# Kernel tuning notes

Hardware: AMD Instinct MI355X
Metric: run time of the kernel (lower is better)

The kernel has to match this reference:

```python
import jax, jax.numpy as jnp
import numpy as np

B = 8192
NUM_SAMPLES = 128
RESAMPLE_PADDING = 0.01
F32_EPS = float(np.finfo(np.float32).eps)


def lift_gaussian_diag(d, t_mean, t_var, r_var):
    # d: [B,3]; t_mean/t_var/r_var: [B,S]
    mean = d[..., None, :] * t_mean[..., None]                      # [B,S,3]
    d_mag_sq = jnp.clip(jnp.sum(d ** 2, axis=-1, keepdims=True), 1e-10)
    d_outer_diag = d ** 2
    null_outer_diag = 1.0 - d_outer_diag / d_mag_sq
    cov_diag = (t_var[..., None] * d_outer_diag[..., None, :]
                + r_var[..., None] * null_outer_diag[..., None, :])  # [B,S,3]
    return mean, cov_diag


def conical_frustum_to_gaussian(d, t0, t1, base_radius):
    # stable=True branch of the original code
    mu = (t0 + t1) / 2
    hw = (t1 - t0) / 2
    t_mean = mu + 2 * mu * hw ** 2 / (3 * mu ** 2 + hw ** 2)
    t_var = hw ** 2 / 3 - 4 / 15 * (hw ** 4 * (12 * mu ** 2 - hw ** 2)
                                    / (3 * mu ** 2 + hw ** 2) ** 2)
    r_var = base_radius ** 2 * (mu ** 2 / 4 + 5 / 12 * hw ** 2
                                - 4 / 15 * hw ** 4 / (3 * mu ** 2 + hw ** 2))
    return lift_gaussian_diag(d, t_mean, t_var, r_var)


def cast_rays(t_vals, origins, directions, radii):
    # ray_shape == 'cone', diag == True
    means, covs = conical_frustum_to_gaussian(
        directions, t_vals[..., :-1], t_vals[..., 1:], radii)
    return means + origins[..., None, :], covs


def sorted_piecewise_constant_pdf(bins, weights, num_samples):
    # randomized=False branch; faithful O(n*m) mask-based interval search
    eps = 1e-5
    weight_sum = jnp.sum(weights, axis=-1, keepdims=True)
    padding = jnp.clip(eps - weight_sum, 0)
    weights = weights + padding / weights.shape[-1]
    weight_sum = weight_sum + padding
    pdf = weights / weight_sum
    cdf = jnp.minimum(jnp.cumsum(pdf[..., :-1], axis=-1), 1.0)
    z = jnp.zeros(cdf.shape[:-1] + (1,), cdf.dtype)
    o = jnp.ones(cdf.shape[:-1] + (1,), cdf.dtype)
    cdf = jnp.concatenate([z, cdf, o], axis=-1)                      # [B, nb+1]
    u = jnp.linspace(0.0, 1.0 - F32_EPS, num_samples, dtype=cdf.dtype)
    u = jnp.broadcast_to(u, cdf.shape[:-1] + (num_samples,))         # [B, S]
    mask = u[..., None, :] >= cdf[..., :, None]                      # [B, nb+1, S]

    def find_interval(x):
        x0 = jnp.max(jnp.where(mask, x[..., None], x[..., :1, None]), axis=-2)
        x1 = jnp.min(jnp.where(~mask, x[..., None], x[..., -1:, None]), axis=-2)
        return x0, x1

    bins_g0, bins_g1 = find_interval(bins)
    cdf_g0, cdf_g1 = find_interval(cdf)
    t = jnp.clip(jnp.nan_to_num((u - cdf_g0) / (cdf_g1 - cdf_g0)), 0, 1)
    return bins_g0 + t * (bins_g1 - bins_g0)


def setup_inputs() -> dict:
    key = jax.random.key(0)
    k0, k1, k2, k3 = jax.random.split(key, 4)
    origins = jax.random.normal(k0, (B, 3), dtype=jnp.float32)
    directions = jax.random.normal(k1, (B, 3), dtype=jnp.float32)
    directions = directions / jnp.linalg.norm(directions, axis=-1, keepdims=True)
    radii = 0.001 + 0.01 * jax.random.uniform(k2, (B, 1), dtype=jnp.float32)
    near = 2.0 * jnp.ones((B, 1), dtype=jnp.float32)
    far = 6.0 * jnp.ones((B, 1), dtype=jnp.float32)
    weights = jax.random.uniform(k3, (B, NUM_SAMPLES), dtype=jnp.float32)
    return {"origins": origins, "directions": directions, "radii": radii,
            "near": near, "far": far, "weights": weights}


def reference(origins, directions, radii, near, far, weights):
    # coarse stratified sampling (randomized=False, lindisp=False)
    t = jnp.linspace(0.0, 1.0, NUM_SAMPLES + 1, dtype=jnp.float32)
    t_coarse = near * (1.0 - t) + far * t                            # [B, S+1]
    means_c, covs_c = cast_rays(t_coarse, origins, directions, radii)
    # resample_along_rays: blur weights then inverse-CDF sample
    wpad = jnp.concatenate([weights[..., :1], weights, weights[..., -1:]], axis=-1)
    wmax = jnp.maximum(wpad[..., :-1], wpad[..., 1:])
    wblur = 0.5 * (wmax[..., :-1] + wmax[..., 1:]) + RESAMPLE_PADDING
    t_fine = sorted_piecewise_constant_pdf(t_coarse, wblur, t_coarse.shape[-1])
    means_f, covs_f = cast_rays(t_fine, origins, directions, radii)
    return (t_coarse, means_c, covs_c, t_fine, means_f, covs_f)
```

## Files before the change

### kernel.cpp

```cpp
#include <hip/hip_runtime.h>


constexpr int B_RAYS = 8192;
constexpr int S      = 128;
constexpr int SP1    = 129;
constexpr float F32_EPS = 1.1920928955078125e-07f;
constexpr float USTEP   = (1.0f - F32_EPS) / 128.0f;
constexpr float R_SCALE = 128.0f / (1.0f - F32_EPS);

constexpr long long O_TC = 0;
constexpr long long O_MC = O_TC + (long long)B_RAYS * SP1;
constexpr long long O_CC = O_MC + (long long)B_RAYS * S * 3;
constexpr long long O_TF = O_CC + (long long)B_RAYS * S * 3;
constexpr long long O_MF = O_TF + (long long)B_RAYS * SP1;
constexpr long long O_CF = O_MF + (long long)B_RAYS * S * 3;

typedef float vf4 __attribute__((ext_vector_type(4)));

__device__ __forceinline__ float frcp(float x) { return __builtin_amdgcn_rcpf(x); }

template<int CTRL, int RM>
__device__ __forceinline__ float dpp_addf(float x) {
    int m = __builtin_amdgcn_update_dpp(0, __builtin_bit_cast(int, x),
                                        CTRL, RM, 0xF, true);
    return x + __builtin_bit_cast(float, m);
}
template<int CTRL>
__device__ __forceinline__ float dpp_movf(float x) {
    int m = __builtin_amdgcn_update_dpp(0, __builtin_bit_cast(int, x),
                                        CTRL, 0xF, 0xF, true);
    return __builtin_bit_cast(float, m);
}

__device__ __forceinline__ void st_nt(float* p, float v) {
    __builtin_nontemporal_store(v, p);
}
__device__ __forceinline__ void st_nt4(float* p, float4 v) {
    __builtin_nontemporal_store(__builtin_bit_cast(vf4, v),
                                reinterpret_cast<vf4*>(p));
}

__device__ __forceinline__ void frustum(float t0, float t1, float rad2,
                                        float& tm, float& tv, float& rv)
{
    float mu  = 0.5f * (t0 + t1);
    float hw  = 0.5f * (t1 - t0);
    float mu2 = mu * mu, hw2 = hw * hw, hw4 = hw2 * hw2;
    float den  = fmaf(3.0f, mu2, hw2);
    float rden = frcp(den);
    tm = fmaf(2.0f * mu * hw2, rden, mu);
    tv = hw2 * (1.0f / 3.0f)
       - (4.0f / 15.0f) * (hw4 * fmaf(12.0f, mu2, -hw2)) * (rden * rden);
    rv = rad2 * (0.25f * mu2 + (5.0f / 12.0f) * hw2 - (4.0f / 15.0f) * hw4 * rden);
}

__device__ __forceinline__ float sel3(int c, float x, float y, float z)
{
    return (c == 0) ? x : ((c == 1) ? y : z);
}

__device__ __forceinline__ int smin_of(float c)
{
    int s = (int)ceilf(c * R_SCALE);
    s = s < 0 ? 0 : (s > 129 ? 129 : s);
    #pragma unroll
    for (int it = 0; it < 2; ++it)
        if (s > 0 && (float)(s - 1) * USTEP >= c) --s;
    #pragma unroll
    for (int it = 0; it < 2; ++it)
        if (s < 129 && (float)s * USTEP < c) ++s;
    return s;
}

__global__ __launch_bounds__(256) void mipnerf_kernel(
    const float* __restrict__ origins,
    const float* __restrict__ directions,
    const float* __restrict__ radii,
    const float* __restrict__ nearp,
    const float* __restrict__ farp,
    const float* __restrict__ weights,
    float* __restrict__ out)
{
    const int tid = threadIdx.x;
    const int w   = tid >> 6;
    const int l   = tid & 63;
    const int b   = (blockIdx.x << 2) + w;

    __shared__ float4 s_pay[4][132];
    __shared__ float4 s_fr[4][128];

    const float2 wv = *reinterpret_cast<const float2*>(weights + (long long)b * S + 2*l);
    const float ox = origins[3*b+0], oy = origins[3*b+1], oz = origins[3*b+2];
    const float dx = directions[3*b+0], dy = directions[3*b+1], dz = directions[3*b+2];
    const float rad = radii[b];
    const float nv = nearp[b], fv = farp[b];

    const float rad2   = rad * rad;
    const float axx = dx*dx, ayy = dy*dy, azz = dz*dz;
    const float dmag2  = fmaxf(axx + ayy + azz, 1e-10f);
    const float rdmag2 = frcp(dmag2);
    const float nxx = 1.0f - axx * rdmag2;
    const float nyy = 1.0f - ayy * rdmag2;
    const float nzz = 1.0f - azz * rdmag2;

    auto bin = [&](int k) {
        float t = (float)k * (1.0f / 128.0f);
        return nv * (1.0f - t) + fv * t;
    };

    {
        float* ot = out + O_TC + (long long)b * SP1;
        st_nt(ot + l,      bin(l));
        st_nt(ot + l + 64, bin(l + 64));
        if (l == 0) st_nt(ot + 128, bin(128));
    }

    #pragma unroll
    for (int j = 0; j < 2; ++j) {
        int i = l + 64*j;
        float tm, tv, rv;
        frustum(bin(i), bin(i + 1), rad2, tm, tv, rv);
        s_fr[w][i] = make_float4(tm, tv, rv, 0.0f);
    }
    __builtin_amdgcn_wave_barrier();

    auto emit_span = [&](int m, float* __restrict__ om, float* __restrict__ oc) {
        int k0 = m + m / 3;
        int r  = 4*m - 3*k0;
        float4 fA = s_fr[w][k0], fB = s_fr[w][k0 + 1];
        float4 mv, cv;
        #pragma unroll
        for (int e = 0; e < 4; ++e) {
            int  rc   = r + e;
            bool useB = rc >= 3;
            int  c    = useB ? rc - 3 : rc;
            float tm = useB ? fB.x : fA.x;
            float tv = useB ? fB.y : fA.y;
            float rv = useB ? fB.z : fA.z;
            (&mv.x)[e] = sel3(c, dx, dy, dz) * tm + sel3(c, ox, oy, oz);
            (&cv.x)[e] = tv * sel3(c, axx, ayy, azz) + rv * sel3(c, nxx, nyy, nzz);
        }
        st_nt4(om + 4*m, mv);
        st_nt4(oc + 4*m, cv);
    };

    {
        float* om = out + O_MC + (long long)b * 384;
        float* oc = out + O_CC + (long long)b * 384;
        emit_span(l, om, oc);
        if (l < 32) emit_span(l + 64, om, oc);
    }

    float wprev = dpp_movf<0x138>(wv.y);  if (l == 0)  wprev = wv.x;
    float wnext = dpp_movf<0x130>(wv.x);  if (l == 63) wnext = wv.y;
    float m0 = fmaxf(wprev, wv.x), m1 = fmaxf(wv.x, wv.y), m2 = fmaxf(wv.y, wnext);
    float wb0 = 0.5f * (m0 + m1) + 0.01f;
    float wb1 = 0.5f * (m1 + m2) + 0.01f;

    float ps = wb0 + wb1;
    float x  = ps;
    x = dpp_addf<0x111, 0xF>(x);
    x = dpp_addf<0x112, 0xF>(x);
    x = dpp_addf<0x114, 0xF>(x);
    x = dpp_addf<0x118, 0xF>(x);
    x = dpp_addf<0x142, 0xA>(x);
    x = dpp_addf<0x143, 0xC>(x);
    float incl  = x;
    float total = __builtin_bit_cast(float,
        __builtin_amdgcn_readlane(__builtin_bit_cast(int, incl), 63));

    float pad   = fmaxf(1e-5f - total, 0.0f);
    float wstot = total + pad;
    float inv   = frcp(wstot);
    float padk  = pad * (1.0f / 128.0f);
    float excl  = incl - ps;

    float Bv = fminf((excl + wb0 + (float)(2*l + 1) * padk) * inv, 1.0f);
    float Cv = (l == 63) ? 1.0f
             : fminf((incl + (float)(2*l + 2) * padk) * inv, 1.0f);
    float Av = dpp_movf<0x138>(Cv);

    int sm0 = smin_of(Av);
    int sm1 = smin_of(Bv);
    int sm2 = smin_of(Cv);
    {
        float4 payA = make_float4(Av, Bv - Av, bin(2*l),     bin(2*l + 1));
        float4 payB = make_float4(Bv, Cv - Bv, bin(2*l + 1), bin(2*l + 2));
        for (int s2 = sm0; s2 < sm1; ++s2) s_pay[w][s2] = payA;
        for (int s2 = sm1; s2 < sm2; ++s2) s_pay[w][s2] = payB;
    }
    __builtin_amdgcn_wave_barrier();

    auto sample_one = [&](int s) -> float {
        float4 p = s_pay[w][s];
        float u  = (float)s * USTEP;
        float tt = (u - p.x) * frcp(p.y);
        if (!(tt == tt)) tt = 0.0f;
        tt = fminf(fmaxf(tt, 0.0f), 1.0f);
        return p.z + tt * (p.w - p.z);
    };
    float tf0 = sample_one(l);
    float tf1 = sample_one(l + 64);
    float tf2 = sample_one(128);
    {
        float* ot = out + O_TF + (long long)b * SP1;
        st_nt(ot + l,      tf0);
        st_nt(ot + l + 64, tf1);
        if (l == 0) st_nt(ot + 128, tf2);
    }

    float tf1_0 = __builtin_bit_cast(float,
        __builtin_amdgcn_readfirstlane(__builtin_bit_cast(int, tf1)));
    float tA1 = dpp_movf<0x130>(tf0);  if (l == 63) tA1 = tf1_0;
    float tB1 = dpp_movf<0x130>(tf1);  if (l == 63) tB1 = tf2;
    {
        float tm, tv, rv;
        frustum(tf0, tA1, rad2, tm, tv, rv);
        s_fr[w][l] = make_float4(tm, tv, rv, 0.0f);
        frustum(tf1, tB1, rad2, tm, tv, rv);
        s_fr[w][l + 64] = make_float4(tm, tv, rv, 0.0f);
    }
    __builtin_amdgcn_wave_barrier();

    {
        float* om = out + O_MF + (long long)b * 384;
        float* oc = out + O_CF + (long long)b * 384;
        emit_span(l, om, oc);
        if (l < 32) emit_span(l + 64, om, oc);
    }
}

extern "C" void kernel_launch(void* const* d_in, const int* in_sizes, int n_in,
                              void* d_out, int out_size, void* d_ws, size_t ws_size,
                              hipStream_t stream)
{
    const float* origins    = (const float*)d_in[0];
    const float* directions = (const float*)d_in[1];
    const float* radii      = (const float*)d_in[2];
    const float* nearp      = (const float*)d_in[3];
    const float* farp       = (const float*)d_in[4];
    const float* weights    = (const float*)d_in[5];
    float* out = (float*)d_out;

    mipnerf_kernel<<<B_RAYS / 4, 256, 0, stream>>>(
        origins, directions, radii, nearp, farp, weights, out);
}
```

Measured before the change: 17.34 us.

## Recompute frustum moments per output span instead of staging through LDS

Drops the s_fr shared-memory staging of per-interval frustum moments. Each lane now recomputes the two frustum moments it needs from bin values (coarse) or from payload lookups via tf_of (fine). This removes LDS writes and reads and two wave barriers. Av is computed directly instead of taken from a DPP shift, and the coarse output is moved after the CDF computation. The cost is redundant frustum arithmetic and repeated s_pay reads and reciprocals for fine samples.

```diff
diff --git a/kernel.cpp b/kernel.cpp
--- a/kernel.cpp
+++ b/kernel.cpp
@@ -87,7 +87,6 @@
     const int b   = (blockIdx.x << 2) + w;
 
     __shared__ float4 s_pay[4][132];
-    __shared__ float4 s_fr[4][128];
 
     const float2 wv = *reinterpret_cast<const float2*>(weights + (long long)b * S + 2*l);
     const float ox = origins[3*b+0], oy = origins[3*b+1], oz = origins[3*b+2];
@@ -113,42 +112,6 @@
         st_nt(ot + l,      bin(l));
         st_nt(ot + l + 64, bin(l + 64));
         if (l == 0) st_nt(ot + 128, bin(128));
-    }
-
-    #pragma unroll
-    for (int j = 0; j < 2; ++j) {
-        int i = l + 64*j;
-        float tm, tv, rv;
-        frustum(bin(i), bin(i + 1), rad2, tm, tv, rv);
-        s_fr[w][i] = make_float4(tm, tv, rv, 0.0f);
-    }
-    __builtin_amdgcn_wave_barrier();
-
-    auto emit_span = [&](int m, float* __restrict__ om, float* __restrict__ oc) {
-        int k0 = m + m / 3;
-        int r  = 4*m - 3*k0;
-        float4 fA = s_fr[w][k0], fB = s_fr[w][k0 + 1];
-        float4 mv, cv;
-        #pragma unroll
-        for (int e = 0; e < 4; ++e) {
-            int  rc   = r + e;
-            bool useB = rc >= 3;
-            int  c    = useB ? rc - 3 : rc;
-            float tm = useB ? fB.x : fA.x;
-            float tv = useB ? fB.y : fA.y;
-            float rv = useB ? fB.z : fA.z;
-            (&mv.x)[e] = sel3(c, dx, dy, dz) * tm + sel3(c, ox, oy, oz);
-            (&cv.x)[e] = tv * sel3(c, axx, ayy, azz) + rv * sel3(c, nxx, nyy, nzz);
-        }
-        st_nt4(om + 4*m, mv);
-        st_nt4(oc + 4*m, cv);
-    };
-
-    {
-        float* om = out + O_MC + (long long)b * 384;
-        float* oc = out + O_CC + (long long)b * 384;
-        emit_span(l, om, oc);
-        if (l < 32) emit_span(l + 64, om, oc);
     }
 
     float wprev = dpp_movf<0x138>(wv.y);  if (l == 0)  wprev = wv.x;
@@ -175,10 +138,11 @@
     float padk  = pad * (1.0f / 128.0f);
     float excl  = incl - ps;
 
+    float Av = (l == 0)  ? 0.0f
+             : fminf((excl + (float)(2*l) * padk) * inv, 1.0f);
     float Bv = fminf((excl + wb0 + (float)(2*l + 1) * padk) * inv, 1.0f);
     float Cv = (l == 63) ? 1.0f
              : fminf((incl + (float)(2*l + 2) * padk) * inv, 1.0f);
-    float Av = dpp_movf<0x138>(Cv);
 
     int sm0 = smin_of(Av);
     int sm1 = smin_of(Bv);
@@ -191,7 +155,42 @@
     }
     __builtin_amdgcn_wave_barrier();
 
-    auto sample_one = [&](int s) -> float {
+    auto emit_span = [&](int m, float t0, float t1, float t2,
+                         float* __restrict__ om, float* __restrict__ oc) {
+        float tmA, tvA, rvA, tmB, tvB, rvB;
+        frustum(t0, t1, rad2, tmA, tvA, rvA);
+        frustum(t1, t2, rad2, tmB, tvB, rvB);
+        int k0 = m + m / 3;
+        int r  = 4*m - 3*k0;
+        float4 mv, cv;
+        #pragma unroll
+        for (int e = 0; e < 4; ++e) {
+            int  rc   = r + e;
+            bool useB = rc >= 3;
+            int  c    = useB ? rc - 3 : rc;
+            float tm = useB ? tmB : tmA;
+            float tv = useB ? tvB : tvA;
+            float rv = useB ? rvB : rvA;
+            (&mv.x)[e] = sel3(c, dx, dy, dz) * tm + sel3(c, ox, oy, oz);
+            (&cv.x)[e] = tv * sel3(c, axx, ayy, azz) + rv * sel3(c, nxx, nyy, nzz);
+        }
+        st_nt4(om + 4*m, mv);
+        st_nt4(oc + 4*m, cv);
+    };
+
+    {
+        float* om = out + O_MC + (long long)b * 384;
+        float* oc = out + O_CC + (long long)b * 384;
+        int k0 = l + l / 3;
+        emit_span(l, bin(k0), bin(k0 + 1), bin(k0 + 2), om, oc);
+        if (l < 32) {
+            int m2s = l + 64;
+            int k0b = m2s + m2s / 3;
+            emit_span(m2s, bin(k0b), bin(k0b + 1), bin(k0b + 2), om, oc);
+        }
+    }
+
+    auto tf_of = [&](int s) -> float {
         float4 p = s_pay[w][s];
         float u  = (float)s * USTEP;
         float tt = (u - p.x) * frcp(p.y);
@@ -199,34 +198,23 @@
         tt = fminf(fmaxf(tt, 0.0f), 1.0f);
         return p.z + tt * (p.w - p.z);
     };
-    float tf0 = sample_one(l);
-    float tf1 = sample_one(l + 64);
-    float tf2 = sample_one(128);
     {
         float* ot = out + O_TF + (long long)b * SP1;
-        st_nt(ot + l,      tf0);
-        st_nt(ot + l + 64, tf1);
-        if (l == 0) st_nt(ot + 128, tf2);
-    }
-
-    float tf1_0 = __builtin_bit_cast(float,
-        __builtin_amdgcn_readfirstlane(__builtin_bit_cast(int, tf1)));
-    float tA1 = dpp_movf<0x130>(tf0);  if (l == 63) tA1 = tf1_0;
-    float tB1 = dpp_movf<0x130>(tf1);  if (l == 63) tB1 = tf2;
-    {
-        float tm, tv, rv;
-        frustum(tf0, tA1, rad2, tm, tv, rv);
-        s_fr[w][l] = make_float4(tm, tv, rv, 0.0f);
-        frustum(tf1, tB1, rad2, tm, tv, rv);
-        s_fr[w][l + 64] = make_float4(tm, tv, rv, 0.0f);
-    }
-    __builtin_amdgcn_wave_barrier();
+        st_nt(ot + l,      tf_of(l));
+        st_nt(ot + l + 64, tf_of(l + 64));
+        if (l == 0) st_nt(ot + 128, tf_of(128));
+    }
 
     {
         float* om = out + O_MF + (long long)b * 384;
         float* oc = out + O_CF + (long long)b * 384;
-        emit_span(l, om, oc);
-        if (l < 32) emit_span(l + 64, om, oc);
+        int k0 = l + l / 3;
+        emit_span(l, tf_of(k0), tf_of(k0 + 1), tf_of(k0 + 2), om, oc);
+        if (l < 32) {
+            int m2s = l + 64;
+            int k0b = m2s + m2s / 3;
+            emit_span(m2s, tf_of(k0b), tf_of(k0b + 1), tf_of(k0b + 2), om, oc);
+        }
     }
 }
 
```

New measurement: 18.91 us. +9.0%, slower.
